# Kernel optimization log

Hardware: AMD Instinct MI355X
Metric: run time of the kernel (lower is better)

The kernel has to match this reference:

```python
import jax, jax.numpy as jnp
import numpy as np

INPUT, HIDDEN, OUTPUT = 512, 1024, 512
B, T = 256, 512

def setup_inputs() -> dict:
    key = jax.random.key(0)
    ks = jax.random.split(key, 15)
    def lin(k, fin, fout):
        bound = 1.0 / np.sqrt(fin)
        kw, kb = jax.random.split(k)
        W = jax.random.uniform(kw, (fout, fin), jnp.float32, -bound, bound)
        b = jax.random.uniform(kb, (fout,), jnp.float32, -bound, bound)
        return W, b
    x = jax.random.normal(ks[0], (B, T, INPUT), jnp.float32)
    Wxr, bxr = lin(ks[1], INPUT, HIDDEN)
    Whr, bhr = lin(ks[2], HIDDEN, HIDDEN)
    Wxc, bxc = lin(ks[3], INPUT, HIDDEN)
    Whc, bhc = lin(ks[4], HIDDEN, HIDDEN)
    Wxz, bxz = lin(ks[5], INPUT, HIDDEN)
    Whz, bhz = lin(ks[6], HIDDEN, HIDDEN)
    Wo, bo = lin(ks[7], HIDDEN, OUTPUT)
    return {"x": x, "Wxr": Wxr, "bxr": bxr, "Whr": Whr, "bhr": bhr,
            "Wxc": Wxc, "bxc": bxc, "Whc": Whc, "bhc": bhc,
            "Wxz": Wxz, "bxz": bxz, "Whz": Whz, "bhz": bhz,
            "Wo": Wo, "bo": bo}

def reference(x, Wxr, bxr, Whr, bhr, Wxc, bxc, Whc, bhc, Wxz, bxz, Whz, bhz, Wo, bo):
    # Precompute all input-to-gate projections in one big GEMM each: [B,T,H]
    xr = jnp.einsum('bti,hi->bth', x, Wxr) + bxr
    xc = jnp.einsum('bti,hi->bth', x, Wxc) + bxc
    xz = jnp.einsum('bti,hi->bth', x, Wxz) + bxz
    # time-major for scan: [T,B,H]
    xs = (xr.transpose(1, 0, 2), xc.transpose(1, 0, 2), xz.transpose(1, 0, 2))

    h0 = jnp.zeros((x.shape[0], Whr.shape[0]), x.dtype)

    def step(h, xt):
        xr_t, xc_t, xz_t = xt
        r = jax.nn.sigmoid(xr_t + h @ Whr.T + bhr)
        c = jnp.tanh(xc_t + r * (h @ Whc.T + bhc))
        z = jax.nn.sigmoid(xz_t + h @ Whz.T + bhz)
        h_new = (1.0 - z) * h + z * c
        return h_new, None

    h_final, _ = jax.lax.scan(step, h0, xs)
    return h_final @ Wo.T + bo
```

## Files before the change

kernel.cpp:

```cpp
#include <hip/hip_runtime.h>

typedef __attribute__((ext_vector_type(8))) short s16x8;
typedef __attribute__((ext_vector_type(4))) float f32x4;

#define SCOPE_AGENT __HIP_MEMORY_SCOPE_AGENT

static __device__ __forceinline__ unsigned short f2bf(float f) {
    unsigned u = __float_as_uint(f);
    u = (u + 0x7fffu + ((u >> 16) & 1u)) >> 16;
    return (unsigned short)u;
}

static __device__ __forceinline__ unsigned ld_sc1(const unsigned* p) {
    return __hip_atomic_load(p, __ATOMIC_RELAXED, SCOPE_AGENT);
}
static __device__ __forceinline__ void st_sc1(unsigned* p, unsigned v) {
    __hip_atomic_store(p, v, __ATOMIC_RELAXED, SCOPE_AGENT);
}

__global__ void k_cast_bf16(const float* __restrict__ src,
                            unsigned short* __restrict__ dst, int n4) {
    int i = blockIdx.x * blockDim.x + threadIdx.x;
    int stride = gridDim.x * blockDim.x;
    for (; i < n4; i += stride) {
        float4 v = reinterpret_cast<const float4*>(src)[i];
        ushort4 o;
        o.x = f2bf(v.x); o.y = f2bf(v.y); o.z = f2bf(v.z); o.w = f2bf(v.w);
        reinterpret_cast<ushort4*>(dst)[i] = o;
    }
}

__global__ __launch_bounds__(256, 1) void k_gru(
    const unsigned short* __restrict__ x16,
    const unsigned short* __restrict__ wh,
    const unsigned short* __restrict__ wx,
    const unsigned short* __restrict__ wo,
    const float* __restrict__ bxr_, const float* __restrict__ bhr_,
    const float* __restrict__ bxc_, const float* __restrict__ bhc_,
    const float* __restrict__ bxz_, const float* __restrict__ bhz_,
    const float* __restrict__ bo_,
    unsigned short* __restrict__ h16a,
    unsigned short* __restrict__ h16b,
    unsigned* __restrict__ slots,
    float* __restrict__ out)
{
    extern __shared__ unsigned short lds[];

    const int tid = threadIdx.x;
    const int bid = blockIdx.x;
    const int xcd = bid & 7;
    const int rb  = xcd >> 1;
    const int jt  = ((bid >> 3) << 1) | (xcd & 1);
    const int b0  = rb * 64;
    const int j0  = jt * 16;

    for (int i = 0; i < 36; ++i) {
        int gidx = i * 256 + tid;
        int rr = gidx / 192;
        int gc = gidx - rr * 192;
        int k  = gc << 3;
        int gate = rr >> 4;
        int j = j0 + (rr & 15);
        const unsigned short* src =
            (k < 1024) ? (wh + ((size_t)gate << 20) + ((size_t)j << 10) + k)
                       : (wx + (size_t)gate * 524288 + ((size_t)j << 9) + (k - 1024));
        s16x8 v = *reinterpret_cast<const s16x8*>(src);
        int boff = ((rr * 192 + gc) << 4) ^ ((rr & 15) << 4);
        *reinterpret_cast<s16x8*>(reinterpret_cast<char*>(lds) + boff) = v;
    }
    __syncthreads();

    const int lane = tid & 63;
    const int wv   = tid >> 6;
    const int l15  = lane & 15;
    const int lk   = lane >> 4;

    const int b   = b0 + wv * 16 + l15;
    const int jq  = j0 + lk * 4;
    const int swz = l15 << 4;
    const int rbase0 = (l15)      * 192 + lk;
    const int rbase1 = (16 + l15) * 192 + lk;
    const int rbase2 = (32 + l15) * 192 + lk;

    float bR[4], bZ[4], bCh[4], bCx[4];
#pragma unroll
    for (int e = 0; e < 4; ++e) {
        int j = jq + e;
        bR[e]  = bxr_[j] + bhr_[j];
        bZ[e]  = bxz_[j] + bhz_[j];
        bCh[e] = bhc_[j];
        bCx[e] = bxc_[j];
    }

    float hreg[4] = {0.f, 0.f, 0.f, 0.f};
    char* lb = reinterpret_cast<char*>(lds);
    const unsigned short* xrowbase = x16 + (size_t)b * 262144 + lk * 8;
    unsigned* myflag  = &slots[(rb << 6) + jt];
    unsigned* gflags  = &slots[rb << 6];

    f32x4 xR = {0.f,0.f,0.f,0.f}, xZ = {0.f,0.f,0.f,0.f}, xC = {0.f,0.f,0.f,0.f};
    {
        s16x8 xf[16];
#pragma unroll
        for (int kk = 0; kk < 16; ++kk)
            xf[kk] = *reinterpret_cast<const s16x8*>(xrowbase + kk * 32);
#pragma unroll
        for (int kk = 0; kk < 16; ++kk) {
            s16x8 w0 = *reinterpret_cast<s16x8*>(lb + (((rbase0 + (kk + 32) * 4) << 4) ^ swz));
            s16x8 w1 = *reinterpret_cast<s16x8*>(lb + (((rbase1 + (kk + 32) * 4) << 4) ^ swz));
            s16x8 w2 = *reinterpret_cast<s16x8*>(lb + (((rbase2 + (kk + 32) * 4) << 4) ^ swz));
            xR = __builtin_amdgcn_mfma_f32_16x16x32_bf16(w0, xf[kk], xR, 0, 0, 0);
            xC = __builtin_amdgcn_mfma_f32_16x16x32_bf16(w1, xf[kk], xC, 0, 0, 0);
            xZ = __builtin_amdgcn_mfma_f32_16x16x32_bf16(w2, xf[kk], xZ, 0, 0, 0);
        }
    }

    unsigned short* hc = h16a;
    unsigned short* hn = h16b;

    for (int t = 0; t < 512; ++t) {
        if (wv == 0) {
            const unsigned tgt = (unsigned)t;
            for (;;) {
                unsigned v = ld_sc1(&gflags[lane]);
                if (__all((int)(v >= tgt))) break;
                __builtin_amdgcn_s_sleep(1);
            }
        }
        __syncthreads();
        asm volatile("" ::: "memory");

        s16x8 hf[32];
        const unsigned short* hrow = hc + ((size_t)b << 10) + lk * 8;
#pragma unroll
        for (int kk = 0; kk < 32; ++kk)
            hf[kk] = *reinterpret_cast<const s16x8*>(hrow + kk * 32);

        s16x8 xfn[16];
        if (t < 511) {
            const unsigned short* axn = xrowbase + (size_t)(t + 1) * 512;
#pragma unroll
            for (int kk = 0; kk < 16; ++kk)
                xfn[kk] = *reinterpret_cast<const s16x8*>(axn + kk * 32);
        }

        f32x4 aR = xR, aZ = xZ, aCx = xC;
        f32x4 aCh = {0.f,0.f,0.f,0.f};
#pragma unroll
        for (int kk = 0; kk < 32; ++kk) {
            s16x8 w0 = *reinterpret_cast<s16x8*>(lb + (((rbase0 + kk * 4) << 4) ^ swz));
            s16x8 w1 = *reinterpret_cast<s16x8*>(lb + (((rbase1 + kk * 4) << 4) ^ swz));
            s16x8 w2 = *reinterpret_cast<s16x8*>(lb + (((rbase2 + kk * 4) << 4) ^ swz));
            aR  = __builtin_amdgcn_mfma_f32_16x16x32_bf16(w0, hf[kk], aR, 0, 0, 0);
            aCh = __builtin_amdgcn_mfma_f32_16x16x32_bf16(w1, hf[kk], aCh, 0, 0, 0);
            aZ  = __builtin_amdgcn_mfma_f32_16x16x32_bf16(w2, hf[kk], aZ, 0, 0, 0);
        }

        unsigned long long pack = 0ull;
#pragma unroll
        for (int e = 0; e < 4; ++e) {
            float r   = __builtin_amdgcn_rcpf(1.f + __expf(-(aR[e] + bR[e])));
            float zg  = __builtin_amdgcn_rcpf(1.f + __expf(-(aZ[e] + bZ[e])));
            float u2  = aCx[e] + bCx[e] + r * (aCh[e] + bCh[e]);
            float cg  = 1.f - 2.f * __builtin_amdgcn_rcpf(__expf(2.f * u2) + 1.f);
            float hnv = (1.f - zg) * hreg[e] + zg * cg;
            hreg[e] = hnv;
            pack |= (unsigned long long)f2bf(hnv) << (16 * e);
        }
        __hip_atomic_store(
            reinterpret_cast<unsigned long long*>(hn + ((size_t)b << 10) + jq),
            pack, __ATOMIC_RELAXED, SCOPE_AGENT);

        __syncthreads();
        if (tid == 0) {
            st_sc1(myflag, (unsigned)(t + 1));
            (void)__hip_atomic_load(myflag, __ATOMIC_ACQUIRE, SCOPE_AGENT);
        }

        if (t < 511) {
            xR = {0.f,0.f,0.f,0.f}; xZ = {0.f,0.f,0.f,0.f}; xC = {0.f,0.f,0.f,0.f};
#pragma unroll
            for (int kk = 0; kk < 16; ++kk) {
                s16x8 w0 = *reinterpret_cast<s16x8*>(lb + (((rbase0 + (kk + 32) * 4) << 4) ^ swz));
                s16x8 w1 = *reinterpret_cast<s16x8*>(lb + (((rbase1 + (kk + 32) * 4) << 4) ^ swz));
                s16x8 w2 = *reinterpret_cast<s16x8*>(lb + (((rbase2 + (kk + 32) * 4) << 4) ^ swz));
                xR = __builtin_amdgcn_mfma_f32_16x16x32_bf16(w0, xfn[kk], xR, 0, 0, 0);
                xC = __builtin_amdgcn_mfma_f32_16x16x32_bf16(w1, xfn[kk], xC, 0, 0, 0);
                xZ = __builtin_amdgcn_mfma_f32_16x16x32_bf16(w2, xfn[kk], xZ, 0, 0, 0);
            }
        }

        unsigned short* tmp = hc; hc = hn; hn = tmp;
    }

    if (wv == 0) {
        for (;;) {
            unsigned v = ld_sc1(&gflags[lane]);
            if (__all((int)(v >= 512u))) break;
            __builtin_amdgcn_s_sleep(1);
        }
        if (tid == 0)
            (void)__hip_atomic_load(myflag, __ATOMIC_ACQUIRE, SCOPE_AGENT);
    }
    __syncthreads();
    asm volatile("" ::: "memory");

    const int ocol  = jt * 8 + l15;
    const int ocolc = (l15 < 8) ? ocol : (jt * 8 + 7);
    f32x4 aO = {0.f,0.f,0.f,0.f};
    const unsigned short* hrow = hc + ((size_t)b << 10) + lk * 8;
    const unsigned short* bw = wo + ((size_t)ocolc << 10) + lk * 8;
#pragma unroll
    for (int kk = 0; kk < 32; ++kk) {
        s16x8 hv = *reinterpret_cast<const s16x8*>(hrow + kk * 32);
        s16x8 wb = *reinterpret_cast<const s16x8*>(bw + kk * 32);
        aO = __builtin_amdgcn_mfma_f32_16x16x32_bf16(hv, wb, aO, 0, 0, 0);
    }
    if (l15 < 8) {
        const float bov = bo_[ocol];
#pragma unroll
        for (int e = 0; e < 4; ++e) {
            out[((size_t)(b0 + wv * 16 + lk * 4 + e) << 9) + ocol] = aO[e] + bov;
        }
    }
}

extern "C" void kernel_launch(void* const* d_in, const int* in_sizes, int n_in,
                              void* d_out, int out_size, void* d_ws, size_t ws_size,
                              hipStream_t stream) {
    const float* x   = (const float*)d_in[0];
    const float* Wxr = (const float*)d_in[1];
    const float* bxr = (const float*)d_in[2];
    const float* Whr = (const float*)d_in[3];
    const float* bhr = (const float*)d_in[4];
    const float* Wxc = (const float*)d_in[5];
    const float* bxc = (const float*)d_in[6];
    const float* Whc = (const float*)d_in[7];
    const float* bhc = (const float*)d_in[8];
    const float* Wxz = (const float*)d_in[9];
    const float* bxz = (const float*)d_in[10];
    const float* Whz = (const float*)d_in[11];
    const float* bhz = (const float*)d_in[12];
    const float* Wo  = (const float*)d_in[13];
    const float* bo  = (const float*)d_in[14];

    char* ws = (char*)d_ws;
    unsigned short* x16  = (unsigned short*)(ws);
    unsigned short* wh   = (unsigned short*)(ws + 134217728);
    unsigned short* wx   = (unsigned short*)(ws + 140509184);
    unsigned short* wo16 = (unsigned short*)(ws + 143654912);
    unsigned short* h16a = (unsigned short*)(ws + 144703488);
    unsigned short* h16b = (unsigned short*)(ws + 145227776);
    unsigned*       slots= (unsigned*)(ws + 145752064);

    auto cast = [&](const float* s, unsigned short* d, int n) {
        int n4 = n >> 2;
        int blocks = (n4 + 255) / 256;
        if (blocks > 4096) blocks = 4096;
        k_cast_bf16<<<blocks, 256, 0, stream>>>(s, d, n4);
    };
    cast(x,   x16, 67108864);
    cast(Whr, wh,            1048576);
    cast(Whc, wh + 1048576,  1048576);
    cast(Whz, wh + 2097152,  1048576);
    cast(Wxr, wx,            524288);
    cast(Wxc, wx + 524288,   524288);
    cast(Wxz, wx + 1048576,  524288);
    cast(Wo,  wo16,          524288);

    hipMemsetAsync(h16a, 0, 524288, stream);
    hipMemsetAsync(slots, 0, 1024, stream);

    hipFuncSetAttribute(reinterpret_cast<const void*>(k_gru),
                        hipFuncAttributeMaxDynamicSharedMemorySize, 147456);
    k_gru<<<dim3(256), dim3(256), 147456, stream>>>(
        x16, wh, wx, wo16, bxr, bhr, bxc, bhc, bxz, bhz, bo,
        h16a, h16b, slots, (float*)d_out);
}
```

Measured before the change: 4.738 ms.

## Split recurrent step wait into two half-K flag barriers to overlap compute

The per-step grid barrier is split in two. Waves first wait only for the producer blocks that own the first half of h, and non-zero waves start the first-half MFMAs while wave 0 waits for the second half. After a second block barrier everyone loads and processes the second half of h. The next-step x fragment load moves after the h store to cut register pressure. This adds an extra __syncthreads per step and assumes flags 0-31 cover h columns 0-511, and wave 0 now does more serial work.

```diff
diff --git a/kernel.cpp b/kernel.cpp
--- a/kernel.cpp
+++ b/kernel.cpp
@@ -119,10 +119,10 @@
     unsigned short* hn = h16b;
 
     for (int t = 0; t < 512; ++t) {
+        const unsigned tgt = (unsigned)t;
         if (wv == 0) {
-            const unsigned tgt = (unsigned)t;
             for (;;) {
-                unsigned v = ld_sc1(&gflags[lane]);
+                unsigned v = ld_sc1(&gflags[lane & 31]);
                 if (__all((int)(v >= tgt))) break;
                 __builtin_amdgcn_s_sleep(1);
             }
@@ -130,30 +130,59 @@
         __syncthreads();
         asm volatile("" ::: "memory");
 
-        s16x8 hf[32];
+        s16x8 hf[16];
         const unsigned short* hrow = hc + ((size_t)b << 10) + lk * 8;
 #pragma unroll
-        for (int kk = 0; kk < 32; ++kk)
+        for (int kk = 0; kk < 16; ++kk)
             hf[kk] = *reinterpret_cast<const s16x8*>(hrow + kk * 32);
-
-        s16x8 xfn[16];
-        if (t < 511) {
-            const unsigned short* axn = xrowbase + (size_t)(t + 1) * 512;
-#pragma unroll
-            for (int kk = 0; kk < 16; ++kk)
-                xfn[kk] = *reinterpret_cast<const s16x8*>(axn + kk * 32);
-        }
 
         f32x4 aR = xR, aZ = xZ, aCx = xC;
         f32x4 aCh = {0.f,0.f,0.f,0.f};
-#pragma unroll
-        for (int kk = 0; kk < 32; ++kk) {
+
+        if (wv != 0) {
+#pragma unroll
+            for (int kk = 0; kk < 16; ++kk) {
+                s16x8 w0 = *reinterpret_cast<s16x8*>(lb + (((rbase0 + kk * 4) << 4) ^ swz));
+                s16x8 w1 = *reinterpret_cast<s16x8*>(lb + (((rbase1 + kk * 4) << 4) ^ swz));
+                s16x8 w2 = *reinterpret_cast<s16x8*>(lb + (((rbase2 + kk * 4) << 4) ^ swz));
+                aR  = __builtin_amdgcn_mfma_f32_16x16x32_bf16(w0, hf[kk], aR, 0, 0, 0);
+                aCh = __builtin_amdgcn_mfma_f32_16x16x32_bf16(w1, hf[kk], aCh, 0, 0, 0);
+                aZ  = __builtin_amdgcn_mfma_f32_16x16x32_bf16(w2, hf[kk], aZ, 0, 0, 0);
+            }
+        } else {
+            for (;;) {
+                unsigned v = ld_sc1(&gflags[32 + (lane & 31)]);
+                if (__all((int)(v >= tgt))) break;
+                __builtin_amdgcn_s_sleep(1);
+            }
+        }
+        __syncthreads();
+        asm volatile("" ::: "memory");
+
+        s16x8 hg[16];
+#pragma unroll
+        for (int kk = 0; kk < 16; ++kk)
+            hg[kk] = *reinterpret_cast<const s16x8*>(hrow + (kk + 16) * 32);
+
+        if (wv == 0) {
+#pragma unroll
+            for (int kk = 0; kk < 16; ++kk) {
+                s16x8 w0 = *reinterpret_cast<s16x8*>(lb + (((rbase0 + kk * 4) << 4) ^ swz));
+                s16x8 w1 = *reinterpret_cast<s16x8*>(lb + (((rbase1 + kk * 4) << 4) ^ swz));
+                s16x8 w2 = *reinterpret_cast<s16x8*>(lb + (((rbase2 + kk * 4) << 4) ^ swz));
+                aR  = __builtin_amdgcn_mfma_f32_16x16x32_bf16(w0, hf[kk], aR, 0, 0, 0);
+                aCh = __builtin_amdgcn_mfma_f32_16x16x32_bf16(w1, hf[kk], aCh, 0, 0, 0);
+                aZ  = __builtin_amdgcn_mfma_f32_16x16x32_bf16(w2, hf[kk], aZ, 0, 0, 0);
+            }
+        }
+#pragma unroll
+        for (int kk = 16; kk < 32; ++kk) {
             s16x8 w0 = *reinterpret_cast<s16x8*>(lb + (((rbase0 + kk * 4) << 4) ^ swz));
             s16x8 w1 = *reinterpret_cast<s16x8*>(lb + (((rbase1 + kk * 4) << 4) ^ swz));
             s16x8 w2 = *reinterpret_cast<s16x8*>(lb + (((rbase2 + kk * 4) << 4) ^ swz));
-            aR  = __builtin_amdgcn_mfma_f32_16x16x32_bf16(w0, hf[kk], aR, 0, 0, 0);
-            aCh = __builtin_amdgcn_mfma_f32_16x16x32_bf16(w1, hf[kk], aCh, 0, 0, 0);
-            aZ  = __builtin_amdgcn_mfma_f32_16x16x32_bf16(w2, hf[kk], aZ, 0, 0, 0);
+            aR  = __builtin_amdgcn_mfma_f32_16x16x32_bf16(w0, hg[kk - 16], aR, 0, 0, 0);
+            aCh = __builtin_amdgcn_mfma_f32_16x16x32_bf16(w1, hg[kk - 16], aCh, 0, 0, 0);
+            aZ  = __builtin_amdgcn_mfma_f32_16x16x32_bf16(w2, hg[kk - 16], aZ, 0, 0, 0);
         }
 
         unsigned long long pack = 0ull;
@@ -178,6 +207,11 @@
         }
 
         if (t < 511) {
+            s16x8 xfn[16];
+            const unsigned short* axn = xrowbase + (size_t)(t + 1) * 512;
+#pragma unroll
+            for (int kk = 0; kk < 16; ++kk)
+                xfn[kk] = *reinterpret_cast<const s16x8*>(axn + kk * 32);
             xR = {0.f,0.f,0.f,0.f}; xZ = {0.f,0.f,0.f,0.f}; xC = {0.f,0.f,0.f,0.f};
 #pragma unroll
             for (int kk = 0; kk < 16; ++kk) {
```

Result: slower. 5.408 ms (+14.1%).
